# Optimization experiments

Measured on AMD Instinct MI355X. Metric: run time of the kernel, lower is better.

## Reference

```python
import jax, jax.numpy as jnp
import numpy as np

B, SQ, SK, D, H = 4, 2048, 2048, 1024, 16
EPS = 1e-6  # flax LayerNorm default


def layer_norm(x, g, b):
    m = x.mean(-1, keepdims=True)
    var = ((x - m) ** 2).mean(-1, keepdims=True)
    return (x - m) * jax.lax.rsqrt(var + EPS) * g + b


def setup_inputs() -> dict:
    key = jax.random.key(0)
    ks = jax.random.split(key, 16)
    s = 1.0 / np.sqrt(D).astype(np.float32)
    inp = {
        'q': jax.random.normal(ks[0], (B, SQ, D), jnp.float32),
        'k': jax.random.normal(ks[1], (B, SK, D), jnp.float32),
        'v': jax.random.normal(ks[2], (B, SK, D), jnp.float32),
        'mask': jax.random.randint(ks[3], (B, SK), 0, 2).astype(bool),
        'Wq': jax.random.normal(ks[4], (D, D), jnp.float32) * s,
        'bq': jnp.zeros((D,), jnp.float32),
        'Wk': jax.random.normal(ks[5], (D, D), jnp.float32) * s,
        'bk': jnp.zeros((D,), jnp.float32),
        'Wv': jax.random.normal(ks[6], (D, D), jnp.float32) * s,
        'bv': jnp.zeros((D,), jnp.float32),
        'Wo': jax.random.normal(ks[7], (D, D), jnp.float32) * s,
        'bo': jnp.zeros((D,), jnp.float32),
        'g1': jnp.ones((D,), jnp.float32),
        'b1': jnp.zeros((D,), jnp.float32),
        'g2': jnp.ones((D,), jnp.float32),
        'b2': jnp.zeros((D,), jnp.float32),
    }
    return inp


def reference(q, k, v, mask, Wq, bq, Wk, bk, Wv, bv, Wo, bo, g1, b1, g2, b2):
    qp = q @ Wq + bq                      # [B, SQ, D]
    kp = k @ Wk + bk                      # [B, SK, D]
    vp = v @ Wv + bv
    qh = qp.reshape(B, SQ, H, D // H)     # head = slice of last dim (matches scatter)
    kh = kp.reshape(B, SK, H, D // H)
    vh = vp.reshape(B, SK, H, D // H)
    # NOTE: original scales by sqrt(dim_out) (full dim), not head dim
    logits = jnp.einsum('bqhd,bkhd->bhqk', qh, kh) / np.sqrt(D).astype(np.float32)
    m = mask[:, None, None, :]            # [B,1,1,SK] broadcast over heads & queries
    A = jax.nn.softmax(jnp.where(m, logits, -jnp.inf), axis=-1)
    A = jnp.where(jnp.isnan(A), 0.0, A)   # fully-masked rows -> 0 (as in original)
    attn = jnp.einsum('bhqk,bkhd->bqhd', A, vh).reshape(B, SQ, D)  # gather heads
    x = layer_norm(qp + attn, g1, b1)
    out = layer_norm(x + jax.nn.relu(x @ Wo + bo), g2, b2)
    return out
```

## Files before the change

### kernel.cpp

```cpp
#include <hip/hip_runtime.h>

#define B_   4
#define SQS  2048
#define SKS  2048
#define DM   1024
#define H_   16
#define MT   8192

typedef __attribute__((ext_vector_type(8))) short bf16x8;
typedef __attribute__((ext_vector_type(4))) float f32x4;

__device__ __forceinline__ float bf2f(unsigned int u) { return __uint_as_float(u << 16); }
__device__ __forceinline__ unsigned short f2bf(float f) {
  unsigned int u = __float_as_uint(f);
  return (unsigned short)((u + 0x7fffu + ((u >> 16) & 1u)) >> 16);
}
__device__ __forceinline__ unsigned int pk_bf16(float a, float b) {
  return __builtin_amdgcn_perm(__float_as_uint(b) + 0x8000u,
                               __float_as_uint(a) + 0x8000u, 0x07060302u);
}
__device__ __forceinline__ unsigned int pk_trunc(float a, float b) {
  return __builtin_amdgcn_perm(__float_as_uint(b), __float_as_uint(a), 0x07060302u);
}
__device__ __forceinline__ float fexp2(float x) {
#if __has_builtin(__builtin_amdgcn_exp2f)
  return __builtin_amdgcn_exp2f(x);
#else
  return __expf(x * 0.69314718056f);
#endif
}
__device__ __forceinline__ void async16(const void* g, void* l) {
  __builtin_amdgcn_global_load_lds((const __attribute__((address_space(1))) unsigned int*)g,
                                   (__attribute__((address_space(3))) unsigned int*)l,
                                   16, 0, 0);
}
__device__ __forceinline__ void cvt8(uint4 u, float* f) {
  f[0] = bf2f(u.x & 0xffffu); f[1] = bf2f(u.x >> 16);
  f[2] = bf2f(u.y & 0xffffu); f[3] = bf2f(u.y >> 16);
  f[4] = bf2f(u.z & 0xffffu); f[5] = bf2f(u.z >> 16);
  f[6] = bf2f(u.w & 0xffffu); f[7] = bf2f(u.w >> 16);
}

#define KSCALE 0.0450842200f
#define BIAS_UNMASKED 0.0028151213f

__global__ __launch_bounds__(256)
void prep_all(const float* __restrict__ q, const float* __restrict__ k,
              const float* __restrict__ v, const int* __restrict__ mask,
              const float* __restrict__ Wq, const float* __restrict__ Wk,
              const float* __restrict__ Wv, const float* __restrict__ Wo,
              unsigned short* __restrict__ qi, unsigned short* __restrict__ ki,
              unsigned short* __restrict__ vi,
              unsigned short* __restrict__ Wqt, unsigned short* __restrict__ Wkt,
              unsigned short* __restrict__ Wvt, unsigned short* __restrict__ Wot,
              float* __restrict__ mskb)
{
  __shared__ float s[32][33];
  const int bx = blockIdx.x, tid = threadIdx.x;
  if (bx < 2048) {
#pragma unroll 1
    for (int it = 0; it < 12; it++) {
      const int i6 = it * 2048 + bx;
      const int which = i6 >> 13, i = i6 & 8191;
      const float* src = (which == 0) ? q : (which == 1) ? k : v;
      unsigned short* dst = (which == 0) ? qi : (which == 1) ? ki : vi;
      size_t o = ((size_t)i * 256 + tid) * 4;
      float4 f = *(const float4*)(src + o);
      uint2 u;
      u.x = pk_bf16(f.x, f.y);
      u.y = pk_bf16(f.z, f.w);
      *(uint2*)(dst + o) = u;
    }
  } else if (bx < 2560) {
#pragma unroll 1
    for (int t8 = 0; t8 < 8; t8++) {
      const int idx = t8 * 512 + (bx - 2048);
      const int w = idx >> 10, t = idx & 1023;
      const int n0 = (t & 31) * 32, k0 = (t >> 5) * 32;
      const float* W = (w == 0) ? Wq : (w == 1) ? Wk : (w == 2) ? Wv : Wo;
      unsigned short* Wt = (w == 0) ? Wqt : (w == 1) ? Wkt : (w == 2) ? Wvt : Wot;
#pragma unroll
      for (int p = 0; p < 4; p++) {
        int c = p * 256 + tid;
        int r = c >> 5, cc = c & 31;
        s[r][cc] = W[(size_t)(k0 + r) * DM + n0 + cc];
      }
      __syncthreads();
#pragma unroll
      for (int p = 0; p < 4; p++) {
        int c = p * 256 + tid;
        int r = c >> 5, cc = c & 31;
        Wt[(size_t)(n0 + r) * DM + k0 + cc] = f2bf(s[cc][r]);
      }
      __syncthreads();
    }
  } else {
    int i = (bx - 2560) * 256 + tid;
    mskb[i] = mask[i] ? BIAS_UNMASKED : -1e30f;
  }
}

__global__ __launch_bounds__(256)
void qkv_gemm(const unsigned short* __restrict__ A0, const unsigned short* __restrict__ A1,
              const unsigned short* __restrict__ A2,
              const unsigned short* __restrict__ W0, const unsigned short* __restrict__ W1,
              const unsigned short* __restrict__ W2,
              const float* __restrict__ s0, const float* __restrict__ s1,
              const float* __restrict__ s2,
              unsigned short* __restrict__ o0, unsigned short* __restrict__ o1,
              unsigned short* __restrict__ vT)
{
  const int L = blockIdx.x + (blockIdx.y << 3) + (blockIdx.z << 9);
  const int g = L & 7, i5 = L >> 3;
  const int nblk = i5 & 7;
  const int yz = (i5 >> 3) + g * 24;
  const int mblk = yz & 63;
  const int z = yz >> 6;

  const unsigned short* A  = (z == 0) ? A0 : (z == 1) ? A1 : A2;
  const unsigned short* Wt = (z == 0) ? W0 : (z == 1) ? W1 : W2;
  const float* bias        = (z == 0) ? s0 : (z == 1) ? s1 : s2;

  __shared__ short SMEM[2 * 128 * 64];
  short* As = SMEM;
  short* Bs = SMEM + 128 * 64;
  const int tid = threadIdx.x;
  const int m0 = mblk * 128, n0 = nblk * 128;
  const int wave = tid >> 6, ln = tid & 15, qd = (tid & 63) >> 4;
  const int wm = (wave >> 1) * 64, wn = (wave & 1) * 64;

  int srow[4], sgj[4];
#pragma unroll
  for (int u = 0; u < 4; u++) {
    int c = u * 256 + tid;
    srow[u] = c >> 3;
    sgj[u] = ((c & 7) ^ (srow[u] & 7)) * 8;
  }

  f32x4 acc[4][4];
  const f32x4 vzero = {0.f, 0.f, 0.f, 0.f};
#pragma unroll
  for (int i = 0; i < 4; i++)
#pragma unroll
    for (int j = 0; j < 4; j++) acc[i][j] = vzero;

  for (int k0 = 0; k0 < DM; k0 += 64) {
    __syncthreads();
#pragma unroll
    for (int u = 0; u < 4; u++) {
      int c = u * 256 + tid;
      async16(A  + (size_t)(m0 + srow[u]) * DM + k0 + sgj[u], (char*)As + c * 16);
      async16(Wt + (size_t)(n0 + srow[u]) * DM + k0 + sgj[u], (char*)Bs + c * 16);
    }
    __syncthreads();

#pragma unroll
    for (int kk = 0; kk < 2; kk++) {
      const int ch = ((kk * 4 + qd) ^ (ln & 7)) * 8;
      bf16x8 af[4], bfr[4];
#pragma unroll
      for (int i = 0; i < 4; i++)
        af[i] = *(const bf16x8*)(As + (wm + i * 16 + ln) * 64 + ch);
#pragma unroll
      for (int j = 0; j < 4; j++)
        bfr[j] = *(const bf16x8*)(Bs + (wn + j * 16 + ln) * 64 + ch);
#pragma unroll
      for (int i = 0; i < 4; i++)
#pragma unroll
        for (int j = 0; j < 4; j++)
          acc[i][j] = __builtin_amdgcn_mfma_f32_16x16x32_bf16(af[i], bfr[j], acc[i][j], 0, 0, 0);
    }
  }

  if (z != 2) {
    unsigned short* C = (z == 0) ? o0 : o1;
    const float sc = (z == 1) ? KSCALE : 1.0f;
#pragma unroll
    for (int j = 0; j < 4; j++) {
      int col = n0 + wn + j * 16 + ln;
      float bj = bias[col];
#pragma unroll
      for (int i = 0; i < 4; i++) {
        int row = m0 + wm + i * 16 + qd * 4;
#pragma unroll
        for (int r = 0; r < 4; r++)
          C[(size_t)(row + r) * DM + col] = f2bf((acc[i][j][r] + bj) * sc);
      }
    }
  } else {
    __syncthreads();
    short* W = SMEM + (wave << 12);
#pragma unroll
    for (int j = 0; j < 4; j++) {
      int col = n0 + wn + j * 16 + ln;
      float bj = bias[col];
      int d = j * 16 + ln;
#pragma unroll
      for (int i = 0; i < 4; i++) {
        int c = (i & 1) * 8 + qd * 2 + ((i >> 1) & 1);
        int pc = c ^ (ln & 7);
        uint2 u;
        u.x = pk_bf16(acc[i][j][0] + bj, acc[i][j][1] + bj);
        u.y = pk_bf16(acc[i][j][2] + bj, acc[i][j][3] + bj);
        *(uint2*)(W + d * 64 + pc * 4) = u;
      }
    }
    const int h  = 2 * nblk + (wave & 1);
    const int bb = (m0 + wm) >> 11;
    const int kg = (m0 + wm) & 2047;
    const int l  = tid & 63;
    unsigned short* vrow_base = vT + ((size_t)(bb * H_ + h) * 64) * SKS + kg;
#pragma unroll
    for (int it = 0; it < 8; it++) {
      int d = it * 8 + (l >> 3);
      int c2 = (l & 7) * 2;
      int pc0 = c2 ^ (d & 7), pc1 = (c2 + 1) ^ (d & 7);
      uint2 a  = *(const uint2*)(W + d * 64 + pc0 * 4);
      uint2 b2 = *(const uint2*)(W + d * 64 + pc1 * 4);
      uint4 o4 = {a.x, a.y, b2.x, b2.y};
      *(uint4*)(vrow_base + (size_t)d * SKS + c2 * 4) = o4;
    }
  }
}

__global__ __launch_bounds__(256)
void gemm_bf16(const unsigned short* __restrict__ A,
               const unsigned short* __restrict__ Wt,
               const float* __restrict__ bias,
               unsigned short* __restrict__ C,
               int relu)
{
  const int L = blockIdx.x + (blockIdx.y << 3);
  const int g = L & 7, i5 = L >> 3;
  const int nblk = i5 & 7;
  const int mblk = (i5 >> 3) + (g << 3);

  __shared__ short As[128 * 64];
  __shared__ short Bs[128 * 64];
  const int tid = threadIdx.x;
  const int m0 = mblk * 128, n0 = nblk * 128;
  const int wave = tid >> 6, ln = tid & 15, qd = (tid & 63) >> 4;
  const int wm = (wave >> 1) * 64, wn = (wave & 1) * 64;

  int srow[4], sgj[4];
#pragma unroll
  for (int u = 0; u < 4; u++) {
    int c = u * 256 + tid;
    srow[u] = c >> 3;
    sgj[u] = ((c & 7) ^ (srow[u] & 7)) * 8;
  }

  f32x4 acc[4][4];
  const f32x4 vzero = {0.f, 0.f, 0.f, 0.f};
#pragma unroll
  for (int i = 0; i < 4; i++)
#pragma unroll
    for (int j = 0; j < 4; j++) acc[i][j] = vzero;

  for (int k0 = 0; k0 < DM; k0 += 64) {
    __syncthreads();
#pragma unroll
    for (int u = 0; u < 4; u++) {
      int c = u * 256 + tid;
      async16(A  + (size_t)(m0 + srow[u]) * DM + k0 + sgj[u], (char*)As + c * 16);
      async16(Wt + (size_t)(n0 + srow[u]) * DM + k0 + sgj[u], (char*)Bs + c * 16);
    }
    __syncthreads();

#pragma unroll
    for (int kk = 0; kk < 2; kk++) {
      const int ch = ((kk * 4 + qd) ^ (ln & 7)) * 8;
      bf16x8 af[4], bfr[4];
#pragma unroll
      for (int i = 0; i < 4; i++)
        af[i] = *(const bf16x8*)(As + (wm + i * 16 + ln) * 64 + ch);
#pragma unroll
      for (int j = 0; j < 4; j++)
        bfr[j] = *(const bf16x8*)(Bs + (wn + j * 16 + ln) * 64 + ch);
#pragma unroll
      for (int i = 0; i < 4; i++)
#pragma unroll
        for (int j = 0; j < 4; j++)
          acc[i][j] = __builtin_amdgcn_mfma_f32_16x16x32_bf16(af[i], bfr[j], acc[i][j], 0, 0, 0);
    }
  }

#pragma unroll
  for (int j = 0; j < 4; j++) {
    int col = n0 + wn + j * 16 + ln;
    float bj = bias[col];
#pragma unroll
    for (int i = 0; i < 4; i++) {
      int row = m0 + wm + i * 16 + qd * 4;
#pragma unroll
      for (int r = 0; r < 4; r++) {
        float v = acc[i][j][r] + bj;
        if (relu) v = fmaxf(v, 0.f);
        C[(size_t)(row + r) * DM + col] = f2bf(v);
      }
    }
  }
}

__global__ __launch_bounds__(256, 4)
void attn_fwd(const unsigned short* __restrict__ qp,
              const unsigned short* __restrict__ kp,
              const unsigned short* __restrict__ vT,
              const float* __restrict__ maskb,
              unsigned short* __restrict__ O0,
              unsigned short* __restrict__ O1,
              float* __restrict__ lws)
{
  __shared__ __align__(16) short Ks[2][64 * 64];
  __shared__ __align__(16) short Vs[2][64 * 64];
  __shared__ __align__(16) float bias_all[1024];

  const int tid = threadIdx.x;
  const int L = blockIdx.x + (blockIdx.y << 4) + (blockIdx.z << 8);
  const int g = L & 7, i5 = L >> 3;
  const int half = i5 & 1;
  const int qblk = (i5 >> 1) & 15;
  const int bh = (i5 >> 5) + (g << 3);
  const int h = bh & 15, b = bh >> 4;
  const int q0 = qblk * 128;
  const int koff0 = half * (SKS / 2);
  const int wave = tid >> 6, ln = tid & 15, qd = (tid & 63) >> 4;

  int sRow[2], sOff[2];
#pragma unroll
  for (int u = 0; u < 2; u++) {
    int c = u * 256 + tid;
    sRow[u] = c >> 3;
    sOff[u] = ((c & 7) ^ (sRow[u] & 7)) * 8;
  }

  const unsigned short* kbase = kp + (size_t)(b * SKS) * DM + (h << 6);
  const unsigned short* vbase = vT + (size_t)((b * H_ + h) * 64) * SKS;

  *(float4*)(bias_all + tid * 4) = *(const float4*)(maskb + b * SKS + koff0 + tid * 4);

  bf16x8 qf[2][2];
#pragma unroll
  for (int gq = 0; gq < 2; gq++) {
    const unsigned short* qrow =
        qp + (size_t)(b * SQS + q0 + wave * 32 + gq * 16 + ln) * DM + (h << 6);
    qf[gq][0] = *(const bf16x8*)(qrow + qd * 8);
    qf[gq][1] = *(const bf16x8*)(qrow + 32 + qd * 8);
  }

  union { bf16x8 v; unsigned int u[4]; } onesf;
  onesf.u[0] = onesf.u[1] = onesf.u[2] = onesf.u[3] = 0x3F803F80u;

  const f32x4 vzero = {0.f, 0.f, 0.f, 0.f};
  f32x4 oA[2][4], lacc[2];
#pragma unroll
  for (int gq = 0; gq < 2; gq++) {
    lacc[gq] = vzero;
#pragma unroll
    for (int t = 0; t < 4; t++) oA[gq][t] = vzero;
  }

#pragma unroll
  for (int u = 0; u < 2; u++) {
    int c = u * 256 + tid;
    async16(kbase + (size_t)(koff0 + sRow[u]) * DM + sOff[u], (char*)Ks[0] + c * 16);
    async16(vbase + (size_t)sRow[u] * SKS + koff0 + sOff[u], (char*)Vs[0] + c * 16);
  }
  __syncthreads();

  const int NT = SKS / 2 / 64;
  for (int kt = 0; kt < NT; kt++) {
    const int cur = kt & 1;
    if (kt + 1 < NT) {
      const int k1 = koff0 + (kt + 1) * 64;
#pragma unroll
      for (int u = 0; u < 2; u++) {
        int c = u * 256 + tid;
        async16(kbase + (size_t)(k1 + sRow[u]) * DM + sOff[u], (char*)Ks[cur ^ 1] + c * 16);
        async16(vbase + (size_t)sRow[u] * SKS + k1 + sOff[u], (char*)Vs[cur ^ 1] + c * 16);
      }
    }
    const short* Ksb = Ks[cur];
    const short* Vsb = Vs[cur];

    bf16x8 pf[2][2];
#pragma unroll
    for (int gq = 0; gq < 2; gq++) {
      f32x4 sS[4];
      __builtin_amdgcn_s_setprio(1);
#pragma unroll
      for (int t = 0; t < 4; t++) {
        const short* krow = Ksb + (t * 16 + ln) * 64;
        bf16x8 kf0 = *(const bf16x8*)(krow + ((0 + qd) ^ (ln & 7)) * 8);
        bf16x8 kf1 = *(const bf16x8*)(krow + ((4 + qd) ^ (ln & 7)) * 8);
        f32x4 btv = *(const f32x4*)(bias_all + kt * 64 + t * 16 + qd * 4);
        f32x4 a = __builtin_amdgcn_mfma_f32_16x16x32_bf16(kf0, qf[gq][0], btv, 0, 0, 0);
        sS[t]   = __builtin_amdgcn_mfma_f32_16x16x32_bf16(kf1, qf[gq][1], a,   0, 0, 0);
      }
      __builtin_amdgcn_s_setprio(0);
      float p[4][4];
#pragma unroll
      for (int t = 0; t < 4; t++) {
        p[t][0] = fexp2(sS[t][0]);
        p[t][1] = fexp2(sS[t][1]);
        p[t][2] = fexp2(sS[t][2]);
        p[t][3] = fexp2(sS[t][3]);
      }
      union { bf16x8 v; unsigned int u[4]; } P0, P1;
      P0.u[0] = pk_trunc(p[0][0], p[0][1]);
      P0.u[1] = pk_trunc(p[0][2], p[0][3]);
      P0.u[2] = pk_trunc(p[2][0], p[2][1]);
      P0.u[3] = pk_trunc(p[2][2], p[2][3]);
      P1.u[0] = pk_trunc(p[1][0], p[1][1]);
      P1.u[1] = pk_trunc(p[1][2], p[1][3]);
      P1.u[2] = pk_trunc(p[3][0], p[3][1]);
      P1.u[3] = pk_trunc(p[3][2], p[3][3]);
      pf[gq][0] = P0.v;
      pf[gq][1] = P1.v;
      lacc[gq] = __builtin_amdgcn_mfma_f32_16x16x32_bf16(pf[gq][0], onesf.v, lacc[gq], 0, 0, 0);
      lacc[gq] = __builtin_amdgcn_mfma_f32_16x16x32_bf16(pf[gq][1], onesf.v, lacc[gq], 0, 0, 0);
    }

    __builtin_amdgcn_s_setprio(1);
#pragma unroll
    for (int t2 = 0; t2 < 4; t2++) {
      const short* vrow = Vsb + (t2 * 16 + ln) * 64;
      bf16x8 vf0 = *(const bf16x8*)(vrow + (((0 + qd) ^ (ln & 7))) * 8);
      bf16x8 vf1 = *(const bf16x8*)(vrow + (((4 + qd) ^ (ln & 7))) * 8);
#pragma unroll
      for (int gq = 0; gq < 2; gq++) {
        oA[gq][t2] = __builtin_amdgcn_mfma_f32_16x16x32_bf16(pf[gq][0], vf0, oA[gq][t2], 0, 0, 0);
        oA[gq][t2] = __builtin_amdgcn_mfma_f32_16x16x32_bf16(pf[gq][1], vf1, oA[gq][t2], 0, 0, 0);
      }
    }
    __builtin_amdgcn_s_setprio(0);

    __syncthreads();
  }

  unsigned short* obuf = half ? O1 : O0;
  float* lbuf = lws + (size_t)half * (B_ * H_ * SQS);
#pragma unroll
  for (int gq = 0; gq < 2; gq++) {
    int qloc = q0 + wave * 32 + gq * 16 + qd * 4;
    if (ln == 0) {
#pragma unroll
      for (int r = 0; r < 4; r++)
        lbuf[(size_t)(b * H_ + h) * SQS + qloc + r] = lacc[gq][r];
    }
#pragma unroll
    for (int t2 = 0; t2 < 4; t2++)
#pragma unroll
      for (int r = 0; r < 4; r++) {
        size_t idx = (size_t)(b * SQS + qloc + r) * DM + (h << 6) + t2 * 16 + ln;
        obuf[idx] = f2bf(oA[gq][t2][r]);
      }
  }
}

__global__ __launch_bounds__(256)
void ln_merge(const unsigned short* __restrict__ Xa, const unsigned short* __restrict__ O0,
              const unsigned short* __restrict__ O1, const float* __restrict__ lws,
              const float* __restrict__ gamma, const float* __restrict__ beta,
              unsigned short* __restrict__ outb)
{
  const int wv = threadIdx.x >> 6, l = threadIdx.x & 63;
  const int row = blockIdx.x * 4 + wv;
  const int b = row >> 11, q = row & 2047;
  const int hh = l >> 2;
  const size_t lidx = (size_t)(b * H_ + hh) * SQS + q;
  float la = lws[lidx], lb2 = lws[lidx + (size_t)(B_ * H_ * SQS)];
  float lsum = la + lb2;
  float linv = (lsum > 0.f) ? 1.0f / lsum : 0.f;

  const size_t base = (size_t)row * DM + l * 16;
  float fa[16], f0[16], f1[16], v[16];
  cvt8(*(const uint4*)(Xa + base),     fa);
  cvt8(*(const uint4*)(Xa + base + 8), fa + 8);
  cvt8(*(const uint4*)(O0 + base),     f0);
  cvt8(*(const uint4*)(O0 + base + 8), f0 + 8);
  cvt8(*(const uint4*)(O1 + base),     f1);
  cvt8(*(const uint4*)(O1 + base + 8), f1 + 8);
  float s = 0.f, s2 = 0.f;
#pragma unroll
  for (int e = 0; e < 16; e++) {
    v[e] = fa[e] + (f0[e] + f1[e]) * linv;
    s  += v[e];
    s2 += v[e] * v[e];
  }
#pragma unroll
  for (int off = 1; off < 64; off <<= 1) {
    s  += __shfl_xor(s, off);
    s2 += __shfl_xor(s2, off);
  }
  float mean = s * (1.0f / 1024.0f);
  float var  = s2 * (1.0f / 1024.0f) - mean * mean;
  float rstd = rsqrtf(var + 1e-6f);
  const int c = l * 16;
  unsigned int o[8];
#pragma unroll
  for (int e = 0; e < 8; e++) {
    float oa = (v[2 * e]     - mean) * rstd * gamma[c + 2 * e]     + beta[c + 2 * e];
    float ob = (v[2 * e + 1] - mean) * rstd * gamma[c + 2 * e + 1] + beta[c + 2 * e + 1];
    o[e] = pk_bf16(oa, ob);
  }
  uint4 o0v = {o[0], o[1], o[2], o[3]};
  uint4 o1v = {o[4], o[5], o[6], o[7]};
  *(uint4*)(outb + base)     = o0v;
  *(uint4*)(outb + base + 8) = o1v;
}

__global__ __launch_bounds__(256)
void ln_fuse(const unsigned short* __restrict__ Xa, const unsigned short* __restrict__ Xb,
             const float* __restrict__ gamma, const float* __restrict__ beta,
             float* __restrict__ outf)
{
  const int wv = threadIdx.x >> 6, l = threadIdx.x & 63;
  const int row = blockIdx.x * 4 + wv;
  const size_t base = (size_t)row * DM + l * 16;
  float fa[16], fb[16], v[16];
  cvt8(*(const uint4*)(Xa + base),     fa);
  cvt8(*(const uint4*)(Xa + base + 8), fa + 8);
  cvt8(*(const uint4*)(Xb + base),     fb);
  cvt8(*(const uint4*)(Xb + base + 8), fb + 8);
  float s = 0.f, s2 = 0.f;
#pragma unroll
  for (int e = 0; e < 16; e++) {
    v[e] = fa[e] + fb[e];
    s  += v[e];
    s2 += v[e] * v[e];
  }
#pragma unroll
  for (int off = 1; off < 64; off <<= 1) {
    s  += __shfl_xor(s, off);
    s2 += __shfl_xor(s2, off);
  }
  float mean = s * (1.0f / 1024.0f);
  float var  = s2 * (1.0f / 1024.0f) - mean * mean;
  float rstd = rsqrtf(var + 1e-6f);
  const int c = l * 16;
#pragma unroll
  for (int e4 = 0; e4 < 4; e4++) {
    float4 ov;
    ov.x = (v[4 * e4 + 0] - mean) * rstd * gamma[c + 4 * e4 + 0] + beta[c + 4 * e4 + 0];
    ov.y = (v[4 * e4 + 1] - mean) * rstd * gamma[c + 4 * e4 + 1] + beta[c + 4 * e4 + 1];
    ov.z = (v[4 * e4 + 2] - mean) * rstd * gamma[c + 4 * e4 + 2] + beta[c + 4 * e4 + 2];
    ov.w = (v[4 * e4 + 3] - mean) * rstd * gamma[c + 4 * e4 + 3] + beta[c + 4 * e4 + 3];
    *(float4*)(outf + base + 4 * e4) = ov;
  }
}

extern "C" void kernel_launch(void* const* d_in, const int* in_sizes, int n_in,
                              void* d_out, int out_size, void* d_ws, size_t ws_size,
                              hipStream_t stream)
{
  (void)in_sizes; (void)n_in; (void)out_size; (void)ws_size;
  const float* q    = (const float*)d_in[0];
  const float* k    = (const float*)d_in[1];
  const float* v    = (const float*)d_in[2];
  const int*   mask = (const int*)  d_in[3];
  const float* Wq   = (const float*)d_in[4];
  const float* bq   = (const float*)d_in[5];
  const float* Wk   = (const float*)d_in[6];
  const float* bk   = (const float*)d_in[7];
  const float* Wv   = (const float*)d_in[8];
  const float* bv   = (const float*)d_in[9];
  const float* Wo   = (const float*)d_in[10];
  const float* bo   = (const float*)d_in[11];
  const float* g1   = (const float*)d_in[12];
  const float* b1   = (const float*)d_in[13];
  const float* g2   = (const float*)d_in[14];
  const float* b2   = (const float*)d_in[15];

  char* ws = (char*)d_ws;
  const size_t SZ16 = (size_t)16 << 20;
  unsigned short* qi   = (unsigned short*)(ws + 0 * SZ16);
  unsigned short* ki   = (unsigned short*)(ws + 1 * SZ16);
  unsigned short* vi   = (unsigned short*)(ws + 2 * SZ16);
  unsigned short* qpb  = (unsigned short*)(ws + 3 * SZ16);
  unsigned short* kpb  = (unsigned short*)(ws + 4 * SZ16);
  unsigned short* vTb  = (unsigned short*)(ws + 6 * SZ16);
  unsigned short* Wqt  = (unsigned short*)(ws + 7 * SZ16 + ((size_t)0 << 20));
  unsigned short* Wkt  = (unsigned short*)(ws + 7 * SZ16 + ((size_t)2 << 20));
  unsigned short* Wvt  = (unsigned short*)(ws + 7 * SZ16 + ((size_t)4 << 20));
  unsigned short* Wot  = (unsigned short*)(ws + 7 * SZ16 + ((size_t)6 << 20));
  float*          mskb = (float*)         (ws + 7 * SZ16 + ((size_t)8 << 20));
  float*          lws  = (float*)         (ws + 7 * SZ16 + ((size_t)9 << 20));
  unsigned short* O0b  = qi;
  unsigned short* O1b  = vi;
  unsigned short* xb   = ki;
  unsigned short* hb   = vTb;

  prep_all     <<<2592,             256, 0, stream>>>(q, k, v, mask, Wq, Wk, Wv, Wo,
                                                      qi, ki, vi, Wqt, Wkt, Wvt, Wot, mskb);

  qkv_gemm     <<<dim3(8, 64, 3),   256, 0, stream>>>(qi, ki, vi, Wqt, Wkt, Wvt,
                                                      bq, bk, bv, qpb, kpb, vTb);

  attn_fwd     <<<dim3(16, 16, 8),  256, 0, stream>>>(qpb, kpb, vTb, mskb, O0b, O1b, lws);

  ln_merge     <<<2048,             256, 0, stream>>>(qpb, O0b, O1b, lws, g1, b1, xb);
  gemm_bf16    <<<dim3(8, 64),      256, 0, stream>>>(xb, Wot, bo, hb, 1);
  ln_fuse      <<<2048,             256, 0, stream>>>(xb, hb, g2, b2, (float*)d_out);
}
```

Before: 360.6 us.

## Compact unmasked keys and values to skip masked tiles in attention

Builds a per-batch list of unmasked key positions in the prep kernel, then a new compaction kernel gathers only those K rows and V^T columns into dense buffers padded to 64. Attention then iterates over only the compacted tiles, derives the mask bias from the count, and drops the two-way key split and its O1/partial-sum merge. This removes work on masked keys (about half with random masks) at the cost of an extra gather pass and fewer attention blocks. Atomic ordering of indices is nondeterministic but softmax sums are order-independent up to rounding.

```diff
diff --git a/kernel.cpp b/kernel.cpp
--- a/kernel.cpp
+++ b/kernel.cpp
@@ -39,6 +39,9 @@
   f[2] = bf2f(u.y & 0xffffu); f[3] = bf2f(u.y >> 16);
   f[4] = bf2f(u.z & 0xffffu); f[5] = bf2f(u.z >> 16);
   f[6] = bf2f(u.w & 0xffffu); f[7] = bf2f(u.w >> 16);
+}
+__device__ __forceinline__ int colp(int g) {
+  return ((g >> 4) & 1) * 32 + ((g >> 2) & 3) * 8 + ((g >> 5) & 1) * 4 + (g & 3);
 }
 
 #define KSCALE 0.0450842200f
@@ -53,9 +56,10 @@
               unsigned short* __restrict__ vi,
               unsigned short* __restrict__ Wqt, unsigned short* __restrict__ Wkt,
               unsigned short* __restrict__ Wvt, unsigned short* __restrict__ Wot,
-              float* __restrict__ mskb)
+              int* __restrict__ idx, int* __restrict__ cinfo)
 {
   __shared__ float s[32][33];
+  __shared__ int lcnt;
   const int bx = blockIdx.x, tid = threadIdx.x;
   if (bx < 2048) {
 #pragma unroll 1
@@ -74,8 +78,8 @@
   } else if (bx < 2560) {
 #pragma unroll 1
     for (int t8 = 0; t8 < 8; t8++) {
-      const int idx = t8 * 512 + (bx - 2048);
-      const int w = idx >> 10, t = idx & 1023;
+      const int idx2 = t8 * 512 + (bx - 2048);
+      const int w = idx2 >> 10, t = idx2 & 1023;
       const int n0 = (t & 31) * 32, k0 = (t >> 5) * 32;
       const float* W = (w == 0) ? Wq : (w == 1) ? Wk : (w == 2) ? Wv : Wo;
       unsigned short* Wt = (w == 0) ? Wqt : (w == 1) ? Wkt : (w == 2) ? Wvt : Wot;
@@ -95,8 +99,19 @@
       __syncthreads();
     }
   } else {
-    int i = (bx - 2560) * 256 + tid;
-    mskb[i] = mask[i] ? BIAS_UNMASKED : -1e30f;
+    const int b = bx - 2560;
+    if (tid == 0) lcnt = 0;
+    __syncthreads();
+#pragma unroll
+    for (int e = 0; e < 8; e++) {
+      int kk = tid * 8 + e;
+      if (mask[b * SKS + kk]) {
+        int j = atomicAdd(&lcnt, 1);
+        idx[b * SKS + j] = kk;
+      }
+    }
+    __syncthreads();
+    if (tid == 0) cinfo[b] = lcnt;
   }
 }
 
@@ -224,6 +239,54 @@
 }
 
 __global__ __launch_bounds__(256)
+void compact_kv(const unsigned short* __restrict__ kpb,
+                const unsigned short* __restrict__ vTb,
+                const int* __restrict__ idx, const int* __restrict__ cinfo,
+                unsigned short* __restrict__ kpc,
+                unsigned short* __restrict__ vTc)
+{
+  const int wave = threadIdx.x >> 6, ln = threadIdx.x & 63;
+  const int task = blockIdx.x * 4 + wave;
+  if (task < 8192) {
+    const int b = task >> 11, j = task & 2047;
+    const int cnt = cinfo[b];
+    const int pad = (cnt + 63) & ~63;
+    if (j >= pad) return;
+    unsigned short* dst = kpc + ((size_t)b * SKS + j) * DM;
+    if (j < cnt) {
+      const unsigned short* src = kpb + ((size_t)b * SKS + idx[b * SKS + j]) * DM;
+      uint4 a = *(const uint4*)(src + ln * 16);
+      uint4 c = *(const uint4*)(src + ln * 16 + 8);
+      *(uint4*)(dst + ln * 16)     = a;
+      *(uint4*)(dst + ln * 16 + 8) = c;
+    } else {
+      uint4 zz = {0u, 0u, 0u, 0u};
+      *(uint4*)(dst + ln * 16)     = zz;
+      *(uint4*)(dst + ln * 16 + 8) = zz;
+    }
+  } else {
+    const int t2 = task - 8192;
+    const int b = t2 >> 10;
+    const int cnt = cinfo[b];
+    const int pad = (cnt + 63) & ~63;
+    const unsigned short* src = vTb + (size_t)t2 * SKS;
+    unsigned short* dst = vTc + (size_t)t2 * SKS;
+    const int cl = colp(ln);
+    const int* idxb = idx + b * SKS;
+#pragma unroll 1
+    for (int j0 = 0; j0 < pad; j0 += 64) {
+      int j = j0 + ln;
+      unsigned short v = 0;
+      if (j < cnt) {
+        int kk = idxb[j];
+        v = src[(kk & ~63) + colp(kk & 63)];
+      }
+      dst[j0 + cl] = v;
+    }
+  }
+}
+
+__global__ __launch_bounds__(256)
 void gemm_bf16(const unsigned short* __restrict__ A,
                const unsigned short* __restrict__ Wt,
                const float* __restrict__ bias,
@@ -304,27 +367,26 @@
 
 __global__ __launch_bounds__(256, 4)
 void attn_fwd(const unsigned short* __restrict__ qp,
-              const unsigned short* __restrict__ kp,
-              const unsigned short* __restrict__ vT,
-              const float* __restrict__ maskb,
+              const unsigned short* __restrict__ kpc,
+              const unsigned short* __restrict__ vTc,
+              const int* __restrict__ cinfo,
               unsigned short* __restrict__ O0,
-              unsigned short* __restrict__ O1,
               float* __restrict__ lws)
 {
   __shared__ __align__(16) short Ks[2][64 * 64];
   __shared__ __align__(16) short Vs[2][64 * 64];
-  __shared__ __align__(16) float bias_all[1024];
 
   const int tid = threadIdx.x;
   const int L = blockIdx.x + (blockIdx.y << 4) + (blockIdx.z << 8);
   const int g = L & 7, i5 = L >> 3;
-  const int half = i5 & 1;
-  const int qblk = (i5 >> 1) & 15;
-  const int bh = (i5 >> 5) + (g << 3);
+  const int qblk = i5 & 15;
+  const int bh = (i5 >> 4) + (g << 3);
   const int h = bh & 15, b = bh >> 4;
   const int q0 = qblk * 128;
-  const int koff0 = half * (SKS / 2);
   const int wave = tid >> 6, ln = tid & 15, qd = (tid & 63) >> 4;
+
+  const int cnt = cinfo[b];
+  const int NT = (cnt + 63) >> 6;
 
   int sRow[2], sOff[2];
 #pragma unroll
@@ -334,10 +396,8 @@
     sOff[u] = ((c & 7) ^ (sRow[u] & 7)) * 8;
   }
 
-  const unsigned short* kbase = kp + (size_t)(b * SKS) * DM + (h << 6);
-  const unsigned short* vbase = vT + (size_t)((b * H_ + h) * 64) * SKS;
-
-  *(float4*)(bias_all + tid * 4) = *(const float4*)(maskb + b * SKS + koff0 + tid * 4);
+  const unsigned short* kbase = kpc + (size_t)(b * SKS) * DM + (h << 6);
+  const unsigned short* vbase = vTc + (size_t)((b * H_ + h) * 64) * SKS;
 
   bf16x8 qf[2][2];
 #pragma unroll
@@ -363,16 +423,16 @@
 #pragma unroll
   for (int u = 0; u < 2; u++) {
     int c = u * 256 + tid;
-    async16(kbase + (size_t)(koff0 + sRow[u]) * DM + sOff[u], (char*)Ks[0] + c * 16);
-    async16(vbase + (size_t)sRow[u] * SKS + koff0 + sOff[u], (char*)Vs[0] + c * 16);
+    async16(kbase + (size_t)sRow[u] * DM + sOff[u], (char*)Ks[0] + c * 16);
+    async16(vbase + (size_t)sRow[u] * SKS + sOff[u], (char*)Vs[0] + c * 16);
   }
   __syncthreads();
 
-  const int NT = SKS / 2 / 64;
+#pragma unroll 1
   for (int kt = 0; kt < NT; kt++) {
     const int cur = kt & 1;
     if (kt + 1 < NT) {
-      const int k1 = koff0 + (kt + 1) * 64;
+      const int k1 = (kt + 1) * 64;
 #pragma unroll
       for (int u = 0; u < 2; u++) {
         int c = u * 256 + tid;
@@ -393,7 +453,12 @@
         const short* krow = Ksb + (t * 16 + ln) * 64;
         bf16x8 kf0 = *(const bf16x8*)(krow + ((0 + qd) ^ (ln & 7)) * 8);
         bf16x8 kf1 = *(const bf16x8*)(krow + ((4 + qd) ^ (ln & 7)) * 8);
-        f32x4 btv = *(const f32x4*)(bias_all + kt * 64 + t * 16 + qd * 4);
+        int jb = kt * 64 + t * 16 + qd * 4;
+        f32x4 btv;
+        btv[0] = (jb + 0 < cnt) ? BIAS_UNMASKED : -1e30f;
+        btv[1] = (jb + 1 < cnt) ? BIAS_UNMASKED : -1e30f;
+        btv[2] = (jb + 2 < cnt) ? BIAS_UNMASKED : -1e30f;
+        btv[3] = (jb + 3 < cnt) ? BIAS_UNMASKED : -1e30f;
         f32x4 a = __builtin_amdgcn_mfma_f32_16x16x32_bf16(kf0, qf[gq][0], btv, 0, 0, 0);
         sS[t]   = __builtin_amdgcn_mfma_f32_16x16x32_bf16(kf1, qf[gq][1], a,   0, 0, 0);
       }
@@ -438,29 +503,27 @@
     __syncthreads();
   }
 
-  unsigned short* obuf = half ? O1 : O0;
-  float* lbuf = lws + (size_t)half * (B_ * H_ * SQS);
 #pragma unroll
   for (int gq = 0; gq < 2; gq++) {
     int qloc = q0 + wave * 32 + gq * 16 + qd * 4;
     if (ln == 0) {
 #pragma unroll
       for (int r = 0; r < 4; r++)
-        lbuf[(size_t)(b * H_ + h) * SQS + qloc + r] = lacc[gq][r];
+        lws[(size_t)(b * H_ + h) * SQS + qloc + r] = lacc[gq][r];
     }
 #pragma unroll
     for (int t2 = 0; t2 < 4; t2++)
 #pragma unroll
       for (int r = 0; r < 4; r++) {
-        size_t idx = (size_t)(b * SQS + qloc + r) * DM + (h << 6) + t2 * 16 + ln;
-        obuf[idx] = f2bf(oA[gq][t2][r]);
+        size_t idx2 = (size_t)(b * SQS + qloc + r) * DM + (h << 6) + t2 * 16 + ln;
+        O0[idx2] = f2bf(oA[gq][t2][r]);
       }
   }
 }
 
 __global__ __launch_bounds__(256)
 void ln_merge(const unsigned short* __restrict__ Xa, const unsigned short* __restrict__ O0,
-              const unsigned short* __restrict__ O1, const float* __restrict__ lws,
+              const float* __restrict__ lws,
               const float* __restrict__ gamma, const float* __restrict__ beta,
               unsigned short* __restrict__ outb)
 {
@@ -469,22 +532,19 @@
   const int b = row >> 11, q = row & 2047;
   const int hh = l >> 2;
   const size_t lidx = (size_t)(b * H_ + hh) * SQS + q;
-  float la = lws[lidx], lb2 = lws[lidx + (size_t)(B_ * H_ * SQS)];
-  float lsum = la + lb2;
+  float lsum = lws[lidx];
   float linv = (lsum > 0.f) ? 1.0f / lsum : 0.f;
 
   const size_t base = (size_t)row * DM + l * 16;
-  float fa[16], f0[16], f1[16], v[16];
+  float fa[16], f0[16], v[16];
   cvt8(*(const uint4*)(Xa + base),     fa);
   cvt8(*(const uint4*)(Xa + base + 8), fa + 8);
   cvt8(*(const uint4*)(O0 + base),     f0);
   cvt8(*(const uint4*)(O0 + base + 8), f0 + 8);
-  cvt8(*(const uint4*)(O1 + base),     f1);
-  cvt8(*(const uint4*)(O1 + base + 8), f1 + 8);
   float s = 0.f, s2 = 0.f;
 #pragma unroll
   for (int e = 0; e < 16; e++) {
-    v[e] = fa[e] + (f0[e] + f1[e]) * linv;
+    v[e] = fa[e] + f0[e] * linv;
     s  += v[e];
     s2 += v[e] * v[e];
   }
@@ -579,27 +639,32 @@
   unsigned short* vi   = (unsigned short*)(ws + 2 * SZ16);
   unsigned short* qpb  = (unsigned short*)(ws + 3 * SZ16);
   unsigned short* kpb  = (unsigned short*)(ws + 4 * SZ16);
+  unsigned short* kpc  = (unsigned short*)(ws + 5 * SZ16);
   unsigned short* vTb  = (unsigned short*)(ws + 6 * SZ16);
   unsigned short* Wqt  = (unsigned short*)(ws + 7 * SZ16 + ((size_t)0 << 20));
   unsigned short* Wkt  = (unsigned short*)(ws + 7 * SZ16 + ((size_t)2 << 20));
   unsigned short* Wvt  = (unsigned short*)(ws + 7 * SZ16 + ((size_t)4 << 20));
   unsigned short* Wot  = (unsigned short*)(ws + 7 * SZ16 + ((size_t)6 << 20));
-  float*          mskb = (float*)         (ws + 7 * SZ16 + ((size_t)8 << 20));
+  int*            idxb = (int*)           (ws + 7 * SZ16 + ((size_t)8 << 20));
+  int*            cinfo= idxb + B_ * SKS;
   float*          lws  = (float*)         (ws + 7 * SZ16 + ((size_t)9 << 20));
+  unsigned short* vTc  = vi;
   unsigned short* O0b  = qi;
-  unsigned short* O1b  = vi;
   unsigned short* xb   = ki;
   unsigned short* hb   = vTb;
 
-  prep_all     <<<2592,             256, 0, stream>>>(q, k, v, mask, Wq, Wk, Wv, Wo,
-                                                      qi, ki, vi, Wqt, Wkt, Wvt, Wot, mskb);
+  prep_all     <<<2564,             256, 0, stream>>>(q, k, v, mask, Wq, Wk, Wv, Wo,
+                                                      qi, ki, vi, Wqt, Wkt, Wvt, Wot,
+                                                      idxb, cinfo);
 
   qkv_gemm     <<<dim3(8, 64, 3),   256, 0, stream>>>(qi, ki, vi, Wqt, Wkt, Wvt,
                                                       bq, bk, bv, qpb, kpb, vTb);
 
-  attn_fwd     <<<dim3(16, 16, 8),  256, 0, stream>>>(qpb, kpb, vTb, mskb, O0b, O1b, lws);
-
-  ln_merge     <<<2048,             256, 0, stream>>>(qpb, O0b, O1b, lws, g1, b1, xb);
+  compact_kv   <<<3072,             256, 0, stream>>>(kpb, vTb, idxb, cinfo, kpc, vTc);
+
+  attn_fwd     <<<dim3(16, 16, 4),  256, 0, stream>>>(qpb, kpc, vTc, cinfo, O0b, lws);
+
+  ln_merge     <<<2048,             256, 0, stream>>>(qpb, O0b, lws, g1, b1, xb);
   gemm_bf16    <<<dim3(8, 64),      256, 0, stream>>>(xb, Wot, bo, hb, 1);
   ln_fuse      <<<2048,             256, 0, stream>>>(xb, hb, g2, b2, (float*)d_out);
 }
```

Result: faster. 347.3 us (-3.7%).
